# Kernel optimization log

Measured on AMD Instinct MI355X. Metric: run time of the kernel, lower is better.

The kernel has to match this reference:

```python
import jax, jax.numpy as jnp
import numpy as np

D_MODEL, N_HEADS, LATENT, ROPE = 4096, 128, 512, 64
HEAD_DIM = D_MODEL // N_HEADS  # 32
B, S = 2, 1024


def setup_inputs() -> dict:
    key = jax.random.key(0)
    ks = jax.random.split(key, 9)
    def w(k, i, o):
        return jax.random.normal(k, (i, o), dtype=jnp.float32) * (1.0 / np.sqrt(i))
    return {
        "x": jax.random.normal(ks[0], (B, S, D_MODEL), dtype=jnp.float32),
        "Wq_down": w(ks[1], D_MODEL, LATENT),
        "Wq_up": w(ks[2], LATENT, N_HEADS * HEAD_DIM),
        "Wq_rope": w(ks[3], D_MODEL, N_HEADS * ROPE),
        "Wkv_down": w(ks[4], D_MODEL, LATENT),
        "Wk_up": w(ks[5], LATENT, N_HEADS * HEAD_DIM),
        "Wv_up": w(ks[6], LATENT, N_HEADS * HEAD_DIM),
        "Wk_rope": w(ks[7], D_MODEL, ROPE),
        "Wo": w(ks[8], N_HEADS * HEAD_DIM, D_MODEL),
    }


def reference(x, Wq_down, Wq_up, Wq_rope, Wkv_down, Wk_up, Wv_up, Wk_rope, Wo):
    b, s, _ = x.shape
    # latent down-projections
    c_q = x @ Wq_down                                   # [B,S,latent]
    c_kv = x @ Wkv_down                                 # [B,S,latent]
    # up-projections, reshaped to per-head
    q_c = (c_q @ Wq_up).reshape(b, s, N_HEADS, HEAD_DIM)    # [B,S,H,Dh]
    q_r = (x @ Wq_rope).reshape(b, s, N_HEADS, ROPE)        # [B,S,H,Dr]
    k_c = (c_kv @ Wk_up).reshape(b, s, N_HEADS, HEAD_DIM)   # [B,S,H,Dh]
    v_c = (c_kv @ Wv_up).reshape(b, s, N_HEADS, HEAD_DIM)   # [B,S,H,Dh]
    k_r = x @ Wk_rope                                       # [B,S,Dr] shared over heads
    scale = jnp.asarray((HEAD_DIM + ROPE) ** 0.5, x.dtype)
    # scores = q.k with q=[q_c|q_r], k=[k_c|k_r(broadcast)] -> split the dot product
    scores = (jnp.einsum("bqhd,bkhd->bhqk", q_c, k_c)
              + jnp.einsum("bqhd,bkd->bhqk", q_r, k_r)) / scale  # [B,H,S,S]
    attn = jax.nn.softmax(scores, axis=-1)
    out = jnp.einsum("bhqk,bkhd->bqhd", attn, v_c)          # [B,S,H,Dh]
    out = out.reshape(b, s, N_HEADS * HEAD_DIM)
    return out @ Wo                                         # [B,S,d_model]
```

## Files before the change

kernel.cpp:

```cpp
#include <hip/hip_runtime.h>
#include <hip/hip_bf16.h>
#include <math.h>

#define D_MODEL 4096
#define N_HEADS 128
#define LATENT  512
#define ROPE_D  64
#define HEAD_D  32
#define BATCH   2
#define SEQ     1024
#define NTOK    (BATCH*SEQ)

typedef unsigned short u16;
typedef __attribute__((ext_vector_type(8))) short bf16x8;
typedef __attribute__((ext_vector_type(4))) float f32x4;

__device__ __forceinline__ u16 f2bf(float f) {
    union { float f; unsigned u; } v; v.f = f;
    unsigned r = (v.u + 0x7fffu + ((v.u >> 16) & 1u)) >> 16;
    return (u16)r;
}

__device__ __forceinline__ void gl_lds16(const u16* g, u16* l) {
    __builtin_amdgcn_global_load_lds(
        (const __attribute__((address_space(1))) unsigned int*)g,
        (__attribute__((address_space(3))) unsigned int*)l, 16, 0, 0);
}

__device__ __forceinline__ void castT_tile(const float* __restrict__ W,
                                           u16* __restrict__ Wt,
                                           int K, int N, int jx, int jy,
                                           float (*tile)[33])
{
    const int tid = threadIdx.x;
    const int j0 = jx * 32, i0 = jy * 32;
    {
        int r = tid >> 3, c4 = (tid & 7) << 2;
        float4 v = *(const float4*)(W + (size_t)(i0 + r) * N + j0 + c4);
        tile[r][c4 + 0] = v.x; tile[r][c4 + 1] = v.y;
        tile[r][c4 + 2] = v.z; tile[r][c4 + 3] = v.w;
    }
    __syncthreads();
    {
        int n = tid >> 3, k4 = (tid & 7) << 2;
        u16 o[4] = { f2bf(tile[k4 + 0][n]), f2bf(tile[k4 + 1][n]),
                     f2bf(tile[k4 + 2][n]), f2bf(tile[k4 + 3][n]) };
        *(uint2*)(Wt + (size_t)(j0 + n) * K + i0 + k4) = *(uint2*)o;
    }
}

template<int MODE>
__device__ __forceinline__ void gemm_core(const u16* __restrict__ A,
                                          const u16* __restrict__ Bt,
                                          void* __restrict__ Cout,
                                          int N, int K, int lda, int ldb, int ldc,
                                          int bm, int bn, u16* As, u16* Bs)
{
    const int tid  = threadIdx.x;
    const int lane = tid & 63;
    const int wave = tid >> 6;
    const int wr = wave >> 1, wc = wave & 1;
    const int l15 = lane & 15, lg = lane >> 4;

    f32x4 acc[4][4];
    #pragma unroll
    for (int i = 0; i < 4; ++i)
        #pragma unroll
        for (int j = 0; j < 4; ++j) acc[i][j] = (f32x4){0.f, 0.f, 0.f, 0.f};

    for (int kt = 0; kt < K; kt += 64) {
        __syncthreads();
        #pragma unroll
        for (int i = 0; i < 4; ++i) {
            int f = i * 256 + tid;
            int row = f >> 3, c = f & 7;
            int sc = c ^ (row & 7);
            gl_lds16(A + (size_t)(bm + row) * lda + kt + sc * 8, As + f * 8);
        }
        #pragma unroll
        for (int i = 0; i < 4; ++i) {
            int f = i * 256 + tid;
            int row = f >> 3, c = f & 7;
            int sc = c ^ (row & 7);
            gl_lds16(Bt + (size_t)(bn + row) * ldb + kt + sc * 8, Bs + f * 8);
        }
        __syncthreads();

        #pragma unroll
        for (int t = 0; t < 2; ++t) {
            bf16x8 af[4], bf[4];
            #pragma unroll
            for (int fm = 0; fm < 4; ++fm) {
                int row = wr * 64 + fm * 16 + l15;
                int c = (t * 4 + lg) ^ (row & 7);
                af[fm] = *(const bf16x8*)(As + row * 64 + c * 8);
            }
            #pragma unroll
            for (int fn = 0; fn < 4; ++fn) {
                int row = wc * 64 + fn * 16 + l15;
                int c = (t * 4 + lg) ^ (row & 7);
                bf[fn] = *(const bf16x8*)(Bs + row * 64 + c * 8);
            }
            #pragma unroll
            for (int fm = 0; fm < 4; ++fm)
                #pragma unroll
                for (int fn = 0; fn < 4; ++fn)
                    acc[fm][fn] = __builtin_amdgcn_mfma_f32_16x16x32_bf16(
                        af[fm], bf[fn], acc[fm][fn], 0, 0, 0);
        }
    }

    #pragma unroll
    for (int fm = 0; fm < 4; ++fm)
        #pragma unroll
        for (int fn = 0; fn < 4; ++fn)
            #pragma unroll
            for (int ri = 0; ri < 4; ++ri) {
                int row = bm + wr * 64 + fm * 16 + 4 * lg + ri;
                int col = bn + wc * 64 + fn * 16 + l15;
                if (col < N) {
                    float v = acc[fm][fn][ri];
                    if (MODE == 1) ((float*)Cout)[(size_t)row * ldc + col] = v;
                    else           ((u16*)Cout)[(size_t)row * ldc + col] = f2bf(v);
                }
            }
}

template<int MODE>
__global__ __launch_bounds__(256)
void gemm_bf16(const u16* __restrict__ A, const u16* __restrict__ Bt,
               void* __restrict__ Cout, int N, int K,
               int lda, int ldb, int ldc)
{
    __shared__ __align__(16) u16 As[128 * 64];
    __shared__ __align__(16) u16 Bs[128 * 64];
    const int nwg  = gridDim.x * gridDim.y;
    const int orig = blockIdx.y * gridDim.x + blockIdx.x;
    const int swz  = (orig & 7) * (nwg >> 3) + (orig >> 3);
    const int bm = (swz % gridDim.y) * 128;
    const int bn = (swz / gridDim.y) * 128;
    gemm_core<MODE>(A, Bt, Cout, N, K, lda, ldb, ldc, bm, bn, As, Bs);
}

__global__ __launch_bounds__(256)
void gemm1_fused(const u16* __restrict__ xb, const u16* __restrict__ BigT,
                 u16* __restrict__ C_big,
                 const float* __restrict__ Wk_up, const float* __restrict__ Wv_up,
                 const float* __restrict__ Wq_up,
                 u16* __restrict__ UpT, u16* __restrict__ WuqT)
{
    __shared__ __align__(16) u16 As[128 * 64];
    __shared__ __align__(16) u16 Bs[128 * 64];
    int id = blockIdx.x;
    if (id < 1168) {
        const int swz = (id & 7) * 146 + (id >> 3);
        const int bm = (swz % 16) * 128;
        const int bn = (swz / 16) * 128;
        gemm_core<0>(xb, BigT, C_big, 9344, 4096, 4096, 4096, 9344, bm, bn, As, Bs);
        return;
    }
    id -= 1168;
    float (*tile)[33] = reinterpret_cast<float(*)[33]>(As);
    if (id < 2048) { castT_tile(Wk_up, UpT, 512, 4096, id & 127, id >> 7, tile); return; }
    id -= 2048;
    if (id < 2048) { castT_tile(Wv_up, UpT + (size_t)4096 * 512, 512, 4096, id & 127, id >> 7, tile); return; }
    id -= 2048;
    castT_tile(Wq_up, WuqT, 512, 4096, id & 127, id >> 7, tile);
}

__global__ __launch_bounds__(256)
void prep_kernel(const float* __restrict__ x, u16* __restrict__ xb,
                 const float* __restrict__ Wq_rope, const float* __restrict__ Wq_down,
                 const float* __restrict__ Wkv_down, const float* __restrict__ Wk_rope,
                 u16* __restrict__ BigT)
{
    __shared__ float tile[32][33];
    const int tid = threadIdx.x;
    int id = blockIdx.x;
    if (id < 4096) {
        size_t i = ((size_t)id * 256 + tid) * 8;
        float4 a = *(const float4*)(x + i);
        float4 b = *(const float4*)(x + i + 4);
        u16 o[8] = {f2bf(a.x), f2bf(a.y), f2bf(a.z), f2bf(a.w),
                    f2bf(b.x), f2bf(b.y), f2bf(b.z), f2bf(b.w)};
        *(bf16x8*)(xb + i) = *(bf16x8*)o;
        return;
    }
    id -= 4096;
    if (id < 32768) { castT_tile(Wq_rope, BigT, 4096, 8192, id & 255, id >> 8, tile); return; }
    id -= 32768;
    if (id < 2048) { castT_tile(Wq_down, BigT + (size_t)8192 * 4096, 4096, 512, id & 15, id >> 4, tile); return; }
    id -= 2048;
    if (id < 2048) { castT_tile(Wkv_down, BigT + (size_t)8704 * 4096, 4096, 512, id & 15, id >> 4, tile); return; }
    id -= 2048;
    if (id < 256) { castT_tile(Wk_rope, BigT + (size_t)9216 * 4096, 4096, 64, id & 1, id >> 1, tile); return; }
    id -= 256;
    {
        u16* dst = BigT + ((size_t)9280 + id) * 4096;
        bf16x8 z = (bf16x8){0, 0, 0, 0, 0, 0, 0, 0};
        *(bf16x8*)(dst + tid * 8) = z;
        *(bf16x8*)(dst + 2048 + tid * 8) = z;
    }
}

__global__ __launch_bounds__(256)
void fused2_kernel(const u16* __restrict__ Cbig, const u16* __restrict__ UpT,
                   u16* __restrict__ C2, const u16* __restrict__ WuqT,
                   u16* __restrict__ q_c, const float* __restrict__ Wo,
                   u16* __restrict__ WoT)
{
    __shared__ __align__(16) u16 As[128 * 64];
    __shared__ __align__(16) u16 Bs[128 * 64];
    int id = blockIdx.x;
    if (id < 1024) {
        const int swz = (id & 7) * 128 + (id >> 3);
        const int bm = (swz & 15) * 128, bn = (swz >> 4) * 128;
        gemm_core<0>(Cbig + 8704, UpT, C2, 8192, 512, 9344, 512, 8192, bm, bn, As, Bs);
        return;
    }
    id -= 1024;
    if (id < 512) {
        const int swz = (id & 7) * 64 + (id >> 3);
        const int bm = (swz & 15) * 128, bn = (swz >> 4) * 128;
        gemm_core<0>(Cbig + 8192, WuqT, q_c, 4096, 512, 9344, 512, 4096, bm, bn, As, Bs);
        return;
    }
    id -= 512;
    {
        float (*tile)[33] = reinterpret_cast<float(*)[33]>(As);
        castT_tile(Wo, WoT, 4096, 4096, id & 127, id >> 7, tile);
    }
}

__global__ __launch_bounds__(256)
void vtrans_kernel(const u16* __restrict__ vc, u16* __restrict__ vt)
{
    __shared__ __align__(16) u16 tile[64][72];
    const int tid = threadIdx.x;
    const int c0 = blockIdx.x * 64;
    const int s0 = blockIdx.y * 64;
    const int b  = blockIdx.z;
    #pragma unroll
    for (int it = 0; it < 2; ++it) {
        int e = it * 256 + tid;
        int r = e >> 3, c8 = e & 7;
        *(bf16x8*)&tile[r][c8 * 8] =
            *(const bf16x8*)(vc + (size_t)(b * SEQ + s0 + r) * 8192 + c0 + c8 * 8);
    }
    __syncthreads();
    #pragma unroll
    for (int it = 0; it < 2; ++it) {
        int e = it * 256 + tid;
        int d = e >> 3, c8 = e & 7;
        u16 o[8];
        #pragma unroll
        for (int j = 0; j < 8; ++j) o[j] = tile[c8 * 8 + j][d];
        *(bf16x8*)(vt + (size_t)(b * D_MODEL + c0 + d) * SEQ + s0 + c8 * 8) = *(bf16x8*)o;
    }
}

__global__ __launch_bounds__(256)
void attn_kernel(const u16* __restrict__ q_c, const u16* __restrict__ q_r,
                 const u16* __restrict__ k_c, const u16* __restrict__ k_r,
                 const u16* __restrict__ vt,  u16* __restrict__ attn_out)
{
    __shared__ __align__(16) u16 s_kc[2][64 * 32];
    __shared__ __align__(16) u16 s_kr[2][64 * 64];
    __shared__ __align__(16) u16 s_vt[2][32 * 64];
    __shared__ __align__(16) u16 s_p[4][2][16 * 64];

    const int tid  = threadIdx.x;
    const int lane = tid & 63;
    const int w    = tid >> 6;
    const int l15  = lane & 15, lg = lane >> 4;
    const int q0 = blockIdx.x * 128;
    const int h  = blockIdx.y;
    const int b  = blockIdx.z;
    const size_t bS = (size_t)b * SEQ;
    const int hc = h * HEAD_D;
    const float c2 = 0.1020620726159658f * 1.44269504088896f;

    const int qA = q0 + w * 16 + l15;
    const int qB = qA + 64;
    const bf16x8 qfA0 = *(const bf16x8*)(q_c + (bS + qA) * 4096 + hc + lg * 8);
    const bf16x8 qfA1 = *(const bf16x8*)(q_r + (bS + qA) * 9344 + h * ROPE_D + lg * 8);
    const bf16x8 qfA2 = *(const bf16x8*)(q_r + (bS + qA) * 9344 + h * ROPE_D + 32 + lg * 8);
    const bf16x8 qfB0 = *(const bf16x8*)(q_c + (bS + qB) * 4096 + hc + lg * 8);
    const bf16x8 qfB1 = *(const bf16x8*)(q_r + (bS + qB) * 9344 + h * ROPE_D + lg * 8);
    const bf16x8 qfB2 = *(const bf16x8*)(q_r + (bS + qB) * 9344 + h * ROPE_D + 32 + lg * 8);

    bf16x8 vone;
    {
        short o = (l15 == 0) ? (short)0x3F80 : (short)0;
        vone = (bf16x8){o, o, o, o, o, o, o, o};
    }

    float m2A = -1e30f, m2B = -1e30f;
    f32x4 oaccA[3], oaccB[3];
    #pragma unroll
    for (int i = 0; i < 3; ++i) {
        oaccA[i] = (f32x4){0.f, 0.f, 0.f, 0.f};
        oaccB[i] = (f32x4){0.f, 0.f, 0.f, 0.f};
    }

    auto stage = [&](int buf, int k0) {
        { int f = tid, r = f >> 2, c = f & 3;
          gl_lds16(k_c + (bS + k0 + r) * 8192 + hc + ((c ^ ((r >> 1) & 3)) << 3),
                   &s_kc[buf][f * 8]); }
        #pragma unroll
        for (int it = 0; it < 2; ++it) {
          int f = it * 256 + tid, r = f >> 3, c = f & 7;
          gl_lds16(k_r + (bS + k0 + r) * 9344 + ((c ^ (r & 7)) << 3),
                   &s_kr[buf][f * 8]); }
        { int f = tid, d = f >> 3, c = f & 7;
          gl_lds16(vt + ((size_t)b * D_MODEL + hc + d) * SEQ + k0 + ((c ^ (d & 7)) << 3),
                   &s_vt[buf][f * 8]); }
    };

    stage(0, 0);
    asm volatile("s_waitcnt vmcnt(0)" ::: "memory");
    __builtin_amdgcn_sched_barrier(0);
    __builtin_amdgcn_s_barrier();
    __builtin_amdgcn_sched_barrier(0);

    int cur = 0;
    for (int t = 0; t < SEQ / 64; ++t) {
        if (t + 1 < SEQ / 64) {
            stage(cur ^ 1, (t + 1) * 64);
            asm volatile("s_waitcnt vmcnt(4)" ::: "memory");
        } else {
            asm volatile("s_waitcnt vmcnt(0)" ::: "memory");
        }
        __builtin_amdgcn_sched_barrier(0);
        __builtin_amdgcn_s_barrier();
        __builtin_amdgcn_sched_barrier(0);

        f32x4 scA[4], scB[4];
        #pragma unroll
        for (int fc = 0; fc < 4; ++fc) {
            scA[fc] = (f32x4){0.f, 0.f, 0.f, 0.f};
            scB[fc] = (f32x4){0.f, 0.f, 0.f, 0.f};
        }
        __builtin_amdgcn_s_setprio(1);
        #pragma unroll
        for (int fc = 0; fc < 4; ++fc) {
            int row = fc * 16 + l15;
            bf16x8 kb = *(const bf16x8*)&s_kc[cur][row * 32 + ((lg ^ ((row >> 1) & 3)) << 3)];
            scA[fc] = __builtin_amdgcn_mfma_f32_16x16x32_bf16(kb, qfA0, scA[fc], 0, 0, 0);
            scB[fc] = __builtin_amdgcn_mfma_f32_16x16x32_bf16(kb, qfB0, scB[fc], 0, 0, 0);
        }
        #pragma unroll
        for (int tt = 0; tt < 2; ++tt) {
            bf16x8 qa = tt ? qfA2 : qfA1;
            bf16x8 qb = tt ? qfB2 : qfB1;
            #pragma unroll
            for (int fc = 0; fc < 4; ++fc) {
                int row = fc * 16 + l15;
                bf16x8 kb = *(const bf16x8*)&s_kr[cur][row * 64 + (((tt * 4 + lg) ^ (row & 7)) << 3)];
                scA[fc] = __builtin_amdgcn_mfma_f32_16x16x32_bf16(kb, qa, scA[fc], 0, 0, 0);
                scB[fc] = __builtin_amdgcn_mfma_f32_16x16x32_bf16(kb, qb, scB[fc], 0, 0, 0);
            }
        }
        __builtin_amdgcn_s_setprio(0);

        #pragma unroll
        for (int st = 0; st < 2; ++st) {
            f32x4* sc = st ? scB : scA;
            float& m2 = st ? m2B : m2A;
            f32x4* oacc = st ? oaccB : oaccA;

            float a0 = fmaxf(fmaxf(sc[0][0], sc[0][1]), sc[0][2]);
            float a1 = fmaxf(fmaxf(sc[0][3], sc[1][0]), sc[1][1]);
            float a2 = fmaxf(fmaxf(sc[1][2], sc[1][3]), sc[2][0]);
            float a3 = fmaxf(fmaxf(sc[2][1], sc[2][2]), sc[2][3]);
            float a4 = fmaxf(fmaxf(sc[3][0], sc[3][1]), sc[3][2]);
            float b0 = fmaxf(fmaxf(a0, a1), a2);
            float b1 = fmaxf(fmaxf(a3, a4), sc[3][3]);
            float lmx = fmaxf(b0, b1);
            if (!__all(lmx * c2 <= m2 + 8.f)) {
                float tmx = fmaxf(lmx, __shfl_xor(lmx, 16));
                tmx = fmaxf(tmx, __shfl_xor(tmx, 32));
                float mn = fmaxf(m2, tmx * c2);
                float corr = exp2f(m2 - mn);
                m2 = mn;
                #pragma unroll
                for (int ri = 0; ri < 4; ++ri) {
                    float cr = __shfl(corr, 4 * lg + ri);
                    oacc[0][ri] *= cr; oacc[1][ri] *= cr; oacc[2][ri] *= cr;
                }
            }
            unsigned pk0[4], pk1[4];
            #pragma unroll
            for (int fc = 0; fc < 4; ++fc) {
                float p0 = exp2f(fmaf(sc[fc][0], c2, -m2));
                float p1 = exp2f(fmaf(sc[fc][1], c2, -m2));
                float p2 = exp2f(fmaf(sc[fc][2], c2, -m2));
                float p3 = exp2f(fmaf(sc[fc][3], c2, -m2));
                asm("v_cvt_pk_bf16_f32 %0, %1, %2" : "=v"(pk0[fc]) : "v"(p0), "v"(p1));
                asm("v_cvt_pk_bf16_f32 %0, %1, %2" : "=v"(pk1[fc]) : "v"(p2), "v"(p3));
            }
            #pragma unroll
            for (int fc = 0; fc < 4; ++fc) {
                int ch = (2 * fc + (lg >> 1)) ^ (l15 & 7);
                *(uint2*)&s_p[w][st][l15 * 64 + ch * 8 + 4 * (lg & 1)] =
                    make_uint2(pk0[fc], pk1[fc]);
            }
        }

        __builtin_amdgcn_s_setprio(1);
        #pragma unroll
        for (int t2 = 0; t2 < 2; ++t2) {
            int pofs = (((t2 * 4 + lg) ^ (l15 & 7)) << 3);
            bf16x8 paA = *(const bf16x8*)&s_p[w][0][l15 * 64 + pofs];
            bf16x8 paB = *(const bf16x8*)&s_p[w][1][l15 * 64 + pofs];
            #pragma unroll
            for (int fd = 0; fd < 2; ++fd) {
                int row = fd * 16 + l15;
                bf16x8 vb = *(const bf16x8*)&s_vt[cur][row * 64 + (((t2 * 4 + lg) ^ (row & 7)) << 3)];
                oaccA[fd] = __builtin_amdgcn_mfma_f32_16x16x32_bf16(paA, vb, oaccA[fd], 0, 0, 0);
                oaccB[fd] = __builtin_amdgcn_mfma_f32_16x16x32_bf16(paB, vb, oaccB[fd], 0, 0, 0);
            }
            oaccA[2] = __builtin_amdgcn_mfma_f32_16x16x32_bf16(paA, vone, oaccA[2], 0, 0, 0);
            oaccB[2] = __builtin_amdgcn_mfma_f32_16x16x32_bf16(paB, vone, oaccB[2], 0, 0, 0);
        }
        __builtin_amdgcn_s_setprio(0);

        asm volatile("s_waitcnt lgkmcnt(0)" ::: "memory");
        __builtin_amdgcn_sched_barrier(0);
        __builtin_amdgcn_s_barrier();
        __builtin_amdgcn_sched_barrier(0);
        cur ^= 1;
    }

    #pragma unroll
    for (int ri = 0; ri < 4; ++ri) {
        float lsA = __shfl(oaccA[2][ri], lg << 4);
        float lsB = __shfl(oaccB[2][ri], lg << 4);
        float invA = 1.f / lsA, invB = 1.f / lsB;
        int rowA = q0 + w * 16 + 4 * lg + ri;
        int rowB = rowA + 64;
        attn_out[(bS + rowA) * 4096 + hc + l15]      = f2bf(oaccA[0][ri] * invA);
        attn_out[(bS + rowA) * 4096 + hc + 16 + l15] = f2bf(oaccA[1][ri] * invA);
        attn_out[(bS + rowB) * 4096 + hc + l15]      = f2bf(oaccB[0][ri] * invB);
        attn_out[(bS + rowB) * 4096 + hc + 16 + l15] = f2bf(oaccB[1][ri] * invB);
    }
}

extern "C" void kernel_launch(void* const* d_in, const int* in_sizes, int n_in,
                              void* d_out, int out_size, void* d_ws, size_t ws_size,
                              hipStream_t stream)
{
    (void)in_sizes; (void)n_in; (void)out_size; (void)ws_size;

    const float* x        = (const float*)d_in[0];
    const float* Wq_down  = (const float*)d_in[1];
    const float* Wq_up    = (const float*)d_in[2];
    const float* Wq_rope  = (const float*)d_in[3];
    const float* Wkv_down = (const float*)d_in[4];
    const float* Wk_up    = (const float*)d_in[5];
    const float* Wv_up    = (const float*)d_in[6];
    const float* Wk_rope  = (const float*)d_in[7];
    const float* Wo       = (const float*)d_in[8];

    u16* ws   = (u16*)d_ws;
    u16* xb   = ws;
    u16* BigT = xb + (size_t)8388608;
    u16* UpT  = BigT + (size_t)38797312;
    u16* WuqT = UpT + (size_t)4194304;
    u16* C_big= WuqT + (size_t)2097152;
    u16* C2   = C_big + (size_t)19136512;
    u16* WoT  = BigT;
    u16* vt   = BigT + (size_t)16777216;
    u16* q_c  = BigT + (size_t)25165824;
    u16* attn_out = xb;

    dim3 blk(256);

    hipLaunchKernelGGL(prep_kernel, dim3(41280), blk, 0, stream,
                       x, xb, Wq_rope, Wq_down, Wkv_down, Wk_rope, BigT);
    hipLaunchKernelGGL(gemm1_fused, dim3(1168 + 6144), blk, 0, stream,
                       xb, BigT, C_big, Wk_up, Wv_up, Wq_up, UpT, WuqT);
    hipLaunchKernelGGL(fused2_kernel, dim3(1024 + 512 + 16384), blk, 0, stream,
                       C_big, UpT, C2, WuqT, q_c, Wo, WoT);
    hipLaunchKernelGGL(vtrans_kernel, dim3(64, 16, 2), blk, 0, stream, C2 + 4096, vt);
    hipLaunchKernelGGL(attn_kernel, dim3(8, 128, 2), blk, 0, stream,
                       q_c, C_big, C2, C_big + 9216, vt, attn_out);
    gemm_bf16<1><<<dim3(32, 16), blk, 0, stream>>>(
        attn_out, WoT, d_out, 4096, 4096, 4096, 4096, 4096);
}
```

Measured before the change: 508.6 us.

## Regroup launches to fuse V transpose and interleave PV MFMAs per query subtile

The K/V up-projection GEMM now runs alone in its own launch. A second launch combines the q_c up-projection, the Wo cast-transpose and the V transpose. This drops the separate vtrans launch and lets independent work share one grid. In the attention kernel, the P·V MFMAs now run right after each query half's softmax, using one shared P buffer per wave instead of a double buffer. That cuts LDS use and may allow better instruction interleaving, at the cost of serialising the two halves through the shared P buffer.

```diff
diff --git a/kernel.cpp b/kernel.cpp
--- a/kernel.cpp
+++ b/kernel.cpp
@@ -46,6 +46,31 @@
         u16 o[4] = { f2bf(tile[k4 + 0][n]), f2bf(tile[k4 + 1][n]),
                      f2bf(tile[k4 + 2][n]), f2bf(tile[k4 + 3][n]) };
         *(uint2*)(Wt + (size_t)(j0 + n) * K + i0 + k4) = *(uint2*)o;
+    }
+}
+
+__device__ __forceinline__ void vtrans_tile(const u16* __restrict__ vc,
+                                            u16* __restrict__ vt,
+                                            int c0, int s0, int b, u16* buf)
+{
+    u16 (*tile)[72] = reinterpret_cast<u16(*)[72]>(buf);
+    const int tid = threadIdx.x;
+    #pragma unroll
+    for (int it = 0; it < 2; ++it) {
+        int e = it * 256 + tid;
+        int r = e >> 3, c8 = e & 7;
+        *(bf16x8*)&tile[r][c8 * 8] =
+            *(const bf16x8*)(vc + (size_t)(b * SEQ + s0 + r) * 8192 + c0 + c8 * 8);
+    }
+    __syncthreads();
+    #pragma unroll
+    for (int it = 0; it < 2; ++it) {
+        int e = it * 256 + tid;
+        int d = e >> 3, c8 = e & 7;
+        u16 o[8];
+        #pragma unroll
+        for (int j = 0; j < 8; ++j) o[j] = tile[c8 * 8 + j][d];
+        *(bf16x8*)(vt + (size_t)(b * D_MODEL + c0 + d) * SEQ + s0 + c8 * 8) = *(bf16x8*)o;
     }
 }
 
@@ -204,21 +229,26 @@
 }
 
 __global__ __launch_bounds__(256)
-void fused2_kernel(const u16* __restrict__ Cbig, const u16* __restrict__ UpT,
-                   u16* __restrict__ C2, const u16* __restrict__ WuqT,
-                   u16* __restrict__ q_c, const float* __restrict__ Wo,
-                   u16* __restrict__ WoT)
+void fused3a_kernel(const u16* __restrict__ Cbig, const u16* __restrict__ UpT,
+                    u16* __restrict__ C2)
 {
     __shared__ __align__(16) u16 As[128 * 64];
     __shared__ __align__(16) u16 Bs[128 * 64];
     int id = blockIdx.x;
-    if (id < 1024) {
-        const int swz = (id & 7) * 128 + (id >> 3);
-        const int bm = (swz & 15) * 128, bn = (swz >> 4) * 128;
-        gemm_core<0>(Cbig + 8704, UpT, C2, 8192, 512, 9344, 512, 8192, bm, bn, As, Bs);
-        return;
-    }
-    id -= 1024;
+    const int swz = (id & 7) * 128 + (id >> 3);
+    const int bm = (swz & 15) * 128, bn = (swz >> 4) * 128;
+    gemm_core<0>(Cbig + 8704, UpT, C2, 8192, 512, 9344, 512, 8192, bm, bn, As, Bs);
+}
+
+__global__ __launch_bounds__(256)
+void fused3b_kernel(const u16* __restrict__ Cbig, const u16* __restrict__ WuqT,
+                    u16* __restrict__ q_c, const float* __restrict__ Wo,
+                    u16* __restrict__ WoT, const u16* __restrict__ C2,
+                    u16* __restrict__ vt)
+{
+    __shared__ __align__(16) u16 As[128 * 64];
+    __shared__ __align__(16) u16 Bs[128 * 64];
+    int id = blockIdx.x;
     if (id < 512) {
         const int swz = (id & 7) * 64 + (id >> 3);
         const int bm = (swz & 15) * 128, bn = (swz >> 4) * 128;
@@ -226,36 +256,15 @@
         return;
     }
     id -= 512;
-    {
+    if (id < 16384) {
         float (*tile)[33] = reinterpret_cast<float(*)[33]>(As);
         castT_tile(Wo, WoT, 4096, 4096, id & 127, id >> 7, tile);
-    }
-}
-
-__global__ __launch_bounds__(256)
-void vtrans_kernel(const u16* __restrict__ vc, u16* __restrict__ vt)
-{
-    __shared__ __align__(16) u16 tile[64][72];
-    const int tid = threadIdx.x;
-    const int c0 = blockIdx.x * 64;
-    const int s0 = blockIdx.y * 64;
-    const int b  = blockIdx.z;
-    #pragma unroll
-    for (int it = 0; it < 2; ++it) {
-        int e = it * 256 + tid;
-        int r = e >> 3, c8 = e & 7;
-        *(bf16x8*)&tile[r][c8 * 8] =
-            *(const bf16x8*)(vc + (size_t)(b * SEQ + s0 + r) * 8192 + c0 + c8 * 8);
-    }
-    __syncthreads();
-    #pragma unroll
-    for (int it = 0; it < 2; ++it) {
-        int e = it * 256 + tid;
-        int d = e >> 3, c8 = e & 7;
-        u16 o[8];
-        #pragma unroll
-        for (int j = 0; j < 8; ++j) o[j] = tile[c8 * 8 + j][d];
-        *(bf16x8*)(vt + (size_t)(b * D_MODEL + c0 + d) * SEQ + s0 + c8 * 8) = *(bf16x8*)o;
+        return;
+    }
+    id -= 16384;
+    {
+        int c0 = (id & 63) * 64, s0 = ((id >> 6) & 15) * 64, b = id >> 10;
+        vtrans_tile(C2 + 4096, vt, c0, s0, b, As);
     }
 }
 
@@ -267,7 +276,7 @@
     __shared__ __align__(16) u16 s_kc[2][64 * 32];
     __shared__ __align__(16) u16 s_kr[2][64 * 64];
     __shared__ __align__(16) u16 s_vt[2][32 * 64];
-    __shared__ __align__(16) u16 s_p[4][2][16 * 64];
+    __shared__ __align__(16) u16 s_p[4][16 * 64];
 
     const int tid  = threadIdx.x;
     const int lane = tid & 63;
@@ -402,28 +411,23 @@
             #pragma unroll
             for (int fc = 0; fc < 4; ++fc) {
                 int ch = (2 * fc + (lg >> 1)) ^ (l15 & 7);
-                *(uint2*)&s_p[w][st][l15 * 64 + ch * 8 + 4 * (lg & 1)] =
+                *(uint2*)&s_p[w][l15 * 64 + ch * 8 + 4 * (lg & 1)] =
                     make_uint2(pk0[fc], pk1[fc]);
             }
-        }
-
-        __builtin_amdgcn_s_setprio(1);
-        #pragma unroll
-        for (int t2 = 0; t2 < 2; ++t2) {
-            int pofs = (((t2 * 4 + lg) ^ (l15 & 7)) << 3);
-            bf16x8 paA = *(const bf16x8*)&s_p[w][0][l15 * 64 + pofs];
-            bf16x8 paB = *(const bf16x8*)&s_p[w][1][l15 * 64 + pofs];
-            #pragma unroll
-            for (int fd = 0; fd < 2; ++fd) {
-                int row = fd * 16 + l15;
-                bf16x8 vb = *(const bf16x8*)&s_vt[cur][row * 64 + (((t2 * 4 + lg) ^ (row & 7)) << 3)];
-                oaccA[fd] = __builtin_amdgcn_mfma_f32_16x16x32_bf16(paA, vb, oaccA[fd], 0, 0, 0);
-                oaccB[fd] = __builtin_amdgcn_mfma_f32_16x16x32_bf16(paB, vb, oaccB[fd], 0, 0, 0);
-            }
-            oaccA[2] = __builtin_amdgcn_mfma_f32_16x16x32_bf16(paA, vone, oaccA[2], 0, 0, 0);
-            oaccB[2] = __builtin_amdgcn_mfma_f32_16x16x32_bf16(paB, vone, oaccB[2], 0, 0, 0);
-        }
-        __builtin_amdgcn_s_setprio(0);
+            __builtin_amdgcn_s_setprio(1);
+            #pragma unroll
+            for (int t2 = 0; t2 < 2; ++t2) {
+                bf16x8 pa = *(const bf16x8*)&s_p[w][l15 * 64 + (((t2 * 4 + lg) ^ (l15 & 7)) << 3)];
+                #pragma unroll
+                for (int fd = 0; fd < 2; ++fd) {
+                    int row = fd * 16 + l15;
+                    bf16x8 vb = *(const bf16x8*)&s_vt[cur][row * 64 + (((t2 * 4 + lg) ^ (row & 7)) << 3)];
+                    oacc[fd] = __builtin_amdgcn_mfma_f32_16x16x32_bf16(pa, vb, oacc[fd], 0, 0, 0);
+                }
+                oacc[2] = __builtin_amdgcn_mfma_f32_16x16x32_bf16(pa, vone, oacc[2], 0, 0, 0);
+            }
+            __builtin_amdgcn_s_setprio(0);
+        }
 
         asm volatile("s_waitcnt lgkmcnt(0)" ::: "memory");
         __builtin_amdgcn_sched_barrier(0);
@@ -480,9 +484,10 @@
                        x, xb, Wq_rope, Wq_down, Wkv_down, Wk_rope, BigT);
     hipLaunchKernelGGL(gemm1_fused, dim3(1168 + 6144), blk, 0, stream,
                        xb, BigT, C_big, Wk_up, Wv_up, Wq_up, UpT, WuqT);
-    hipLaunchKernelGGL(fused2_kernel, dim3(1024 + 512 + 16384), blk, 0, stream,
-                       C_big, UpT, C2, WuqT, q_c, Wo, WoT);
-    hipLaunchKernelGGL(vtrans_kernel, dim3(64, 16, 2), blk, 0, stream, C2 + 4096, vt);
+    hipLaunchKernelGGL(fused3a_kernel, dim3(1024), blk, 0, stream,
+                       C_big, UpT, C2);
+    hipLaunchKernelGGL(fused3b_kernel, dim3(512 + 16384 + 2048), blk, 0, stream,
+                       C_big, WuqT, q_c, Wo, WoT, C2, vt);
     hipLaunchKernelGGL(attn_kernel, dim3(8, 128, 2), blk, 0, stream,
                        q_c, C_big, C2, C_big + 9216, vt, attn_out);
     gemm_bf16<1><<<dim3(32, 16), blk, 0, stream>>>(
```

New measurement: 516.8 us. Within noise of the previous version (+1.6%).
